# Kernel tuning notes

Hardware: AMD Instinct MI355X
Metric: run time of the kernel (lower is better)

The kernel has to match this reference:

```python
import jax, jax.numpy as jnp
import numpy as np

N = 4096        # batch size (rows)
K = 4           # instances per class -> num_instances in the torch code
D = 256         # embedding dim
MARGIN = 0.5
SAMPLE_KEY = jax.random.key(42)  # fixed key: deterministic stand-in for torch.multinomial


def setup_inputs() -> dict:
    key = jax.random.key(0)
    x = jax.random.normal(key, (N, D), dtype=jnp.float32)
    # L2-normalize like typical metric-learning embeddings so sims are in [-1, 1]
    inputs = x / jnp.linalg.norm(x, axis=1, keepdims=True)
    targets = (jnp.arange(N) // K).astype(jnp.int32)  # P*K batch: equal-size classes
    return {"inputs": inputs, "targets": targets}


def reference(inputs, targets):
    n = inputs.shape[0]
    km1 = K - 1                 # positives per row
    n_neg = n - K               # negatives per row

    sim = inputs @ inputs.T                                   # [n, n]
    same = targets[:, None] == targets[None, :]
    eye = jnp.eye(n, dtype=bool)
    pos_mask = same & ~eye
    neg_mask = ~same

    # masked_select + per-row sort: masked entries -> +inf, ascending sort,
    # keep first count entries (counts are uniform across rows)
    pos_sorted = jnp.sort(jnp.where(pos_mask, sim, jnp.inf), axis=1)[:, :km1]   # [n, K-1]
    neg_sorted = jnp.sort(jnp.where(neg_mask, sim, jnp.inf), axis=1)[:, :n_neg] # [n, n-K]

    pos_d = jnp.mean(pos_sorted)
    neg_d = jnp.mean(neg_sorted)

    # GaussDistribution per row over negatives
    neg_mean = jnp.mean(neg_sorted, axis=1, keepdims=True)
    neg_std = jnp.sqrt(jnp.mean((neg_sorted - neg_mean) ** 2, axis=1, keepdims=True))
    # NOTE: the original uses exp(+(x-mu)^2 / (2 sigma^2)) (no minus sign) -- faithful
    logprob = (neg_sorted - neg_mean) ** 2 / (2.0 * neg_std ** 2)               # [n, n-K]

    # multinomial without replacement ~ Gumbel top-k on log-weights
    gumbel = -jnp.log(-jnp.log(
        jax.random.uniform(SAMPLE_KEY, logprob.shape, minval=1e-20, maxval=1.0)))
    _, neg_idx = jax.lax.top_k(logprob + gumbel, km1)                            # [n, K-1]
    neg_pair = jnp.take_along_axis(neg_sorted, neg_idx, axis=1)                  # [n, K-1]

    pos_loss = jnp.mean(jnp.log1p(jnp.exp(-2.0 * (pos_sorted - MARGIN))), axis=1)
    neg_loss = 0.04 * jnp.mean(jnp.log1p(jnp.exp(50.0 * (neg_pair - MARGIN))), axis=1)
    loss = jnp.sum(pos_loss + neg_loss) / n

    # prec: fraction of rows where hardest positive > hardest sampled negative + 0.05
    c = jnp.sum(pos_sorted[:, -1] > jnp.max(neg_pair, axis=1) + 0.05)
    prec = c.astype(jnp.float32) / n

    return loss, prec, pos_d, neg_d
```

## Files before the change

kernel.cpp:

```cpp
#include <hip/hip_runtime.h>
#include <hip/hip_bf16.h>
#include <cstdint>
#include <cfloat>
#include <math.h>

#define NN 4096
#define DD 256
#define NNEG 4092
#define MARGIN 0.5f
#define NB 3584
#define NW (NB / 2)
#define GTOTAL ((uint32_t)NN * (uint32_t)NNEG)

__device__ __forceinline__ uint32_t rotl32(uint32_t x, int r) {
  return (x << r) | (x >> (32 - r));
}

__device__ __forceinline__ void threefry2x32_42(uint32_t x0, uint32_t x1,
                                                uint32_t& o0, uint32_t& o1) {
  const uint32_t k0 = 0u, k1 = 42u;
  const uint32_t k2 = k0 ^ k1 ^ 0x1BD11BDAu;
  x0 += k0; x1 += k1;
#define TF_R(r) { x0 += x1; x1 = rotl32(x1, r); x1 ^= x0; }
  TF_R(13) TF_R(15) TF_R(26) TF_R(6)
  x0 += k1; x1 += k2 + 1u;
  TF_R(17) TF_R(29) TF_R(16) TF_R(24)
  x0 += k2; x1 += k0 + 2u;
  TF_R(13) TF_R(15) TF_R(26) TF_R(6)
  x0 += k0; x1 += k1 + 3u;
  TF_R(17) TF_R(29) TF_R(16) TF_R(24)
  x0 += k1; x1 += k2 + 4u;
  TF_R(13) TF_R(15) TF_R(26) TF_R(6)
  x0 += k2; x1 += k0 + 5u;
#undef TF_R
  o0 = x0; o1 = x1;
}

__device__ __forceinline__ float gumbel_at(uint32_t f) {
  uint32_t o0, o1;
  threefry2x32_42(0u, f, o0, o1);
  uint32_t bits = o0 ^ o1;
  uint32_t fb = (bits >> 9) | 0x3F800000u;
  float fl = __uint_as_float(fb) - 1.0f;
  float u = fmaxf(1e-20f, fl + 1e-20f);
  return -logf(-logf(u));
}

__device__ __forceinline__ int bucket_of(float v) {
  return (int)fminf(fmaxf((v + 0.28f) * 6400.0f, 0.0f), (float)(NB - 1));
}

#define BT 64
#define NTT (NN / BT)
#define GEMM_BLOCKS (NTT * (NTT + 1) / 2)
#define BK 64
#define LDSS 68
#define GUMBEL_BLOCKS 384

template <int GOFF>
__global__ __launch_bounds__(256) void gemm_gumbel(const float* __restrict__ X,
                                                   float* __restrict__ S,
                                                   float* __restrict__ G) {
  __shared__ float As[BT * LDSS];
  __shared__ float Bs[BT * LDSS];
  const int tid = threadIdx.x;

  if (GOFF > 0 && (int)blockIdx.x < GOFF) {
    uint32_t i = (uint32_t)blockIdx.x * 256u + (uint32_t)tid;
    const uint32_t stride = (uint32_t)GOFF * 256u;
    for (; i < GTOTAL; i += stride) G[i] = gumbel_at(i);
    return;
  }

  const int tx = tid & 15, ty = tid >> 4;

  int b = (int)blockIdx.x - GOFF, bi = 0;
  while (b >= NTT - bi) { b -= NTT - bi; bi++; }
  const int bj = bi + b;
  const int rowBase = bi * BT, colBase = bj * BT;

  float acc[4][4] = {};
  for (int kb = 0; kb < DD; kb += BK) {
#pragma unroll
    for (int it = 0; it < 4; ++it) {
      int idx = tid + 256 * it;
      int r = idx >> 4, c4 = idx & 15;
      float4 av = *(const float4*)(X + (size_t)(rowBase + r) * DD + kb + c4 * 4);
      float4 bv = *(const float4*)(X + (size_t)(colBase + r) * DD + kb + c4 * 4);
      *(float4*)(As + r * LDSS + c4 * 4) = av;
      *(float4*)(Bs + r * LDSS + c4 * 4) = bv;
    }
    __syncthreads();
    for (int k = 0; k < BK; k += 4) {
      float4 a[4], bfr[4];
#pragma unroll
      for (int i = 0; i < 4; ++i) a[i] = *(const float4*)(As + (ty + 16 * i) * LDSS + k);
#pragma unroll
      for (int j = 0; j < 4; ++j) bfr[j] = *(const float4*)(Bs + (tx + 16 * j) * LDSS + k);
#pragma unroll
      for (int i = 0; i < 4; ++i)
#pragma unroll
        for (int j = 0; j < 4; ++j) {
          acc[i][j] += a[i].x * bfr[j].x;
          acc[i][j] += a[i].y * bfr[j].y;
          acc[i][j] += a[i].z * bfr[j].z;
          acc[i][j] += a[i].w * bfr[j].w;
        }
    }
    __syncthreads();
  }
#pragma unroll
  for (int i = 0; i < 4; ++i)
#pragma unroll
    for (int j = 0; j < 4; ++j)
      S[(size_t)(rowBase + ty + 16 * i) * NN + colBase + tx + 16 * j] = acc[i][j];
  if (bi != bj) {
#pragma unroll
    for (int i = 0; i < 4; ++i)
#pragma unroll
      for (int j = 0; j < 4; ++j)
        S[(size_t)(colBase + tx + 16 * j) * NN + rowBase + ty + 16 * i] = acc[i][j];
  }
}

#define INSERT3(sc, v)                                              \
  if ((sc) > s2) {                                                  \
    if ((sc) > s1) {                                                \
      s2 = s1; v2 = v1;                                             \
      if ((sc) > s0) { s1 = s0; v1 = v0; s0 = (sc); v0 = (v); }     \
      else           { s1 = (sc); v1 = (v); }                       \
    } else { s2 = (sc); v2 = (v); }                                 \
  }

template <int USE_G>
__global__ __launch_bounds__(256) void row_kernel(const float* __restrict__ S,
                                                  const float* __restrict__ G,
                                                  float* __restrict__ acc) {
  __shared__ uint32_t histw[NW];
  __shared__ uint32_t offsw[NW];
  __shared__ __align__(16) float sval[NN];
  __shared__ float sh[48];
  __shared__ uint32_t wtot[4];

  const int row = blockIdx.x;
  const int tid = threadIdx.x;
  const int lane = tid & 63, wid = tid >> 6;

#pragma unroll
  for (int i = 0; i < 7; ++i) histw[tid + 256 * i] = 0u;

  const float4* src = (const float4*)(S + (size_t)row * NN);
  const int pslot = row >> 2;
  float vv[16];
#pragma unroll
  for (int it = 0; it < 4; ++it) {
    int slot = tid + 256 * it;
    float4 t4 = src[slot];
    if (slot == pslot) {
      sh[16] = t4.x; sh[17] = t4.y; sh[18] = t4.z; sh[19] = t4.w;
      t4.x = INFINITY; t4.y = INFINITY; t4.z = INFINITY; t4.w = INFINITY;
    }
    vv[4 * it + 0] = t4.x; vv[4 * it + 1] = t4.y;
    vv[4 * it + 2] = t4.z; vv[4 * it + 3] = t4.w;
  }

  float s = 0.0f;
#pragma unroll
  for (int e = 0; e < 16; ++e) if (vv[e] < 1e30f) s += vv[e];
#pragma unroll
  for (int off = 32; off > 0; off >>= 1) s += __shfl_down(s, off, 64);
  if (lane == 0) sh[5 + wid] = s;
  __syncthreads();

#pragma unroll
  for (int e = 0; e < 16; ++e) {
    int b = bucket_of(vv[e]);
    atomicAdd(&histw[b >> 1], 1u << ((b & 1) << 4));
  }
  if (tid == 0) {
    int self = row & 3;
    float p[3]; int m = 0;
#pragma unroll
    for (int c = 0; c < 4; ++c)
      if (c != self) p[m++] = sh[16 + c];
    float t;
    if (p[0] > p[1]) { t = p[0]; p[0] = p[1]; p[1] = t; }
    if (p[1] > p[2]) { t = p[1]; p[1] = p[2]; p[2] = t; }
    if (p[0] > p[1]) { t = p[0]; p[0] = p[1]; p[1] = t; }
    sh[0] = p[0]; sh[1] = p[1]; sh[2] = p[2];
    float tot = sh[5] + sh[6] + sh[7] + sh[8];
    sh[9] = tot;
    sh[3] = tot / (float)NNEG;
  }
  __syncthreads();

  uint32_t hw[7];
  uint32_t s14 = 0;
#pragma unroll
  for (int j = 0; j < 7; ++j) {
    hw[j] = histw[7 * tid + j];
    s14 += (hw[j] & 0xFFFFu) + (hw[j] >> 16);
  }
  uint32_t inc = s14;
#pragma unroll
  for (int off = 1; off < 64; off <<= 1) {
    uint32_t n = __shfl_up(inc, (unsigned)off, 64);
    if (lane >= off) inc += n;
  }
  if (lane == 63) wtot[wid] = inc;

  const float mu = sh[3];
  float q = 0.0f;
#pragma unroll
  for (int e = 0; e < 16; ++e)
    if (vv[e] < 1e30f) { float d = vv[e] - mu; q += d * d; }
#pragma unroll
  for (int off = 32; off > 0; off >>= 1) q += __shfl_down(q, off, 64);
  if (lane == 0) sh[10 + wid] = q;
  __syncthreads();

  uint32_t wbase = 0;
  for (int w = 0; w < wid; ++w) wbase += wtot[w];
  uint32_t run = wbase + inc - s14;
#pragma unroll
  for (int j = 0; j < 7; ++j) {
    uint32_t lo = run; run += hw[j] & 0xFFFFu;
    uint32_t hi = run; run += hw[j] >> 16;
    offsw[7 * tid + j] = lo | (hi << 16);
  }
  if (tid == 0) {
    float var = (sh[10] + sh[11] + sh[12] + sh[13]) / (float)NNEG;
    float sd = sqrtf(var);
    sh[4] = 1.0f / (2.0f * sd * sd);
  }
  __syncthreads();

#pragma unroll
  for (int e = 0; e < 16; ++e) {
    int b = bucket_of(vv[e]);
    uint32_t old = atomicAdd(&offsw[b >> 1], 1u << ((b & 1) << 4));
    uint32_t sl = (old >> ((b & 1) << 4)) & 0xFFFFu;
    sval[sl] = vv[e];
  }
  __syncthreads();

  const float inv2s2 = sh[4];
  const uint32_t fbase = (uint32_t)row * (uint32_t)NNEG;
  const float* __restrict__ Grow = G + fbase;
  float s0 = -FLT_MAX, s1 = -FLT_MAX, s2 = -FLT_MAX;
  float v0 = 0.0f, v1 = 0.0f, v2 = 0.0f;

  float va[16]; uint32_t sten[16];
#pragma unroll
  for (int it = 0; it < 16; ++it) va[it] = sval[tid + 256 * it];
#pragma unroll
  for (int it = 0; it < 16; ++it) {
    float v = va[it];
    uint32_t pk = 0u;
    if (v < 1e30f) {
      int b = bucket_of(v);
      uint32_t sh16 = (uint32_t)((b & 1) << 4);
      uint32_t end = (offsw[b >> 1] >> sh16) & 0xFFFFu;
      uint32_t cb = (histw[b >> 1] >> sh16) & 0xFFFFu;
      pk = (end - cb) | (end << 16);
    }
    sten[it] = pk;
  }

#pragma unroll
  for (int half = 0; half < 2; ++half) {
    float4 w0[8];
#pragma unroll
    for (int j = 0; j < 8; ++j) {
      uint32_t st = sten[half * 8 + j] & 0xFFFFu;
      w0[j] = *(const float4*)(sval + (st & ~3u));
    }
#pragma unroll
    for (int j = 0; j < 8; ++j) {
      const int it = half * 8 + j;
      float v = va[it];
      if (v < 1e30f) {
        const int sl = tid + 256 * it;
        const uint32_t st = sten[it] & 0xFFFFu, en = sten[it] >> 16;
        const uint32_t nb = en - st;
        const uint32_t u0 = st & ~3u;
        int cnt = (int)st;
        {
          float4 w = w0[j];
          cnt += ((u0 + 0 - st) < nb && (w.x < v || (w.x == v && (int)(u0 + 0) < sl))) ? 1 : 0;
          cnt += ((u0 + 1 - st) < nb && (w.y < v || (w.y == v && (int)(u0 + 1) < sl))) ? 1 : 0;
          cnt += ((u0 + 2 - st) < nb && (w.z < v || (w.z == v && (int)(u0 + 2) < sl))) ? 1 : 0;
          cnt += ((u0 + 3 - st) < nb && (w.w < v || (w.w == v && (int)(u0 + 3) < sl))) ? 1 : 0;
        }
        for (uint32_t u = u0 + 4; u < en; u += 4) {
          float4 w = *(const float4*)(sval + u);
          cnt += ((u + 0 - st) < nb && (w.x < v || (w.x == v && (int)(u + 0) < sl))) ? 1 : 0;
          cnt += ((u + 1 - st) < nb && (w.y < v || (w.y == v && (int)(u + 1) < sl))) ? 1 : 0;
          cnt += ((u + 2 - st) < nb && (w.z < v || (w.z == v && (int)(u + 2) < sl))) ? 1 : 0;
          cnt += ((u + 3 - st) < nb && (w.w < v || (w.w == v && (int)(u + 3) < sl))) ? 1 : 0;
        }
        float g = USE_G ? Grow[cnt] : gumbel_at(fbase + (uint32_t)cnt);
        float d = v - mu;
        float sc = d * d * inv2s2 + g;
        INSERT3(sc, v)
      }
    }
  }

#pragma unroll
  for (int dlt = 1; dlt < 64; dlt <<= 1) {
    float t0 = __shfl_xor(s0, dlt, 64), u0 = __shfl_xor(v0, dlt, 64);
    float t1 = __shfl_xor(s1, dlt, 64), u1 = __shfl_xor(v1, dlt, 64);
    float t2 = __shfl_xor(s2, dlt, 64), u2 = __shfl_xor(v2, dlt, 64);
    INSERT3(t0, u0)
    INSERT3(t1, u1)
    INSERT3(t2, u2)
  }
  if (lane == 0) {
    int b0 = 24 + wid * 6;
    sh[b0 + 0] = s0; sh[b0 + 1] = v0;
    sh[b0 + 2] = s1; sh[b0 + 3] = v1;
    sh[b0 + 4] = s2; sh[b0 + 5] = v2;
  }
  __syncthreads();

  if (tid == 0) {
    float g0 = -FLT_MAX, g1 = -FLT_MAX, g2 = -FLT_MAX;
    float w0 = 0.0f, w1 = 0.0f, w2 = 0.0f;
    {
      float s0 = g0, s1 = g1, s2 = g2, v0 = w0, v1 = w1, v2 = w2;
#pragma unroll
      for (int i = 0; i < 12; ++i) {
        float sc = sh[24 + 2 * i], v = sh[24 + 2 * i + 1];
        INSERT3(sc, v)
      }
      g0 = s0; g1 = s1; g2 = s2; w0 = v0; w1 = v1; w2 = v2;
    }
    float negmax = fmaxf(w0, fmaxf(w1, w2));
    float neg_loss = 0.04f * (log1pf(expf(50.0f * (w0 - MARGIN))) +
                              log1pf(expf(50.0f * (w1 - MARGIN))) +
                              log1pf(expf(50.0f * (w2 - MARGIN)))) / 3.0f;
    float p0 = sh[0], p1 = sh[1], p2 = sh[2];
    float pos_loss = (log1pf(expf(-2.0f * (p0 - MARGIN))) +
                      log1pf(expf(-2.0f * (p1 - MARGIN))) +
                      log1pf(expf(-2.0f * (p2 - MARGIN)))) / 3.0f;
    atomicAdd(&acc[0], pos_loss + neg_loss);
    if (p2 > negmax + 0.05f) atomicAdd(&acc[1], 1.0f);
    atomicAdd(&acc[2], p0 + p1 + p2);
    atomicAdd(&acc[3], sh[9]);
  }
}

__global__ void finalize(const float* __restrict__ acc, float* out) {
  if (threadIdx.x == 0 && blockIdx.x == 0) {
    out[0] = acc[0] / 4096.0f;
    out[1] = acc[1] / 4096.0f;
    out[2] = acc[2] / (4096.0f * 3.0f);
    out[3] = acc[3] / (4096.0f * 4092.0f);
  }
}

extern "C" void kernel_launch(void* const* d_in, const int* in_sizes, int n_in,
                              void* d_out, int out_size, void* d_ws, size_t ws_size,
                              hipStream_t stream) {
  (void)in_sizes; (void)n_in; (void)out_size;
  const float* X = (const float*)d_in[0];
  float* S = (float*)d_ws;
  float* acc = (float*)((char*)d_ws + (size_t)NN * NN * 4);
  float* G = (float*)((char*)d_ws + (size_t)NN * NN * 4 + 256);
  const size_t need = (size_t)NN * NN * 4 + 256 + (size_t)GTOTAL * 4;
  const bool have_g = ws_size >= need;

  hipMemsetAsync(acc, 0, 4 * sizeof(float), stream);
  if (have_g) {
    gemm_gumbel<GUMBEL_BLOCKS><<<GUMBEL_BLOCKS + GEMM_BLOCKS, 256, 0, stream>>>(X, S, G);
    row_kernel<1><<<NN, 256, 0, stream>>>(S, G, acc);
  } else {
    gemm_gumbel<0><<<GEMM_BLOCKS, 256, 0, stream>>>(X, S, G);
    row_kernel<0><<<NN, 256, 0, stream>>>(S, G, acc);
  }
  finalize<<<1, 64, 0, stream>>>(acc, (float*)d_out);
}
```

Measured before the change: 375.0 us.

## Enlarge GEMM tiles to 128x128 and optionally move row sort buffer to global

Retiles the similarity GEMM to 128x128 blocks with a K-step of 32 and an 8x8 per-thread register tile. This cuts the number of blocks and the global reloads of X per output, and the Gumbel-generation blocks are moved after the GEMM blocks. The row kernel can now place its bucket-sorted value buffer in a per-row global workspace instead of LDS when the workspace is large enough. That frees about 16KB of LDS per block to allow higher occupancy, at the cost of scattered writes and repeated reads going through the cache hierarchy. The larger register tile raises register pressure in the GEMM.

```diff
diff --git a/kernel.cpp b/kernel.cpp
--- a/kernel.cpp
+++ b/kernel.cpp
@@ -50,12 +50,12 @@
   return (int)fminf(fmaxf((v + 0.28f) * 6400.0f, 0.0f), (float)(NB - 1));
 }
 
-#define BT 64
-#define NTT (NN / BT)
-#define GEMM_BLOCKS (NTT * (NTT + 1) / 2)
-#define BK 64
-#define LDSS 68
-#define GUMBEL_BLOCKS 384
+#define BT 128
+#define NT (NN / BT)
+#define BK 32
+#define LDSS 36
+#define GEMM_BLOCKS (NT * (NT + 1) / 2)
+#define GUMBEL_BLOCKS 240
 
 template <int GOFF>
 __global__ __launch_bounds__(256) void gemm_gumbel(const float* __restrict__ X,
@@ -65,8 +65,8 @@
   __shared__ float Bs[BT * LDSS];
   const int tid = threadIdx.x;
 
-  if (GOFF > 0 && (int)blockIdx.x < GOFF) {
-    uint32_t i = (uint32_t)blockIdx.x * 256u + (uint32_t)tid;
+  if (GOFF > 0 && (int)blockIdx.x >= GEMM_BLOCKS) {
+    uint32_t i = (uint32_t)(blockIdx.x - GEMM_BLOCKS) * 256u + (uint32_t)tid;
     const uint32_t stride = (uint32_t)GOFF * 256u;
     for (; i < GTOTAL; i += stride) G[i] = gumbel_at(i);
     return;
@@ -74,17 +74,17 @@
 
   const int tx = tid & 15, ty = tid >> 4;
 
-  int b = (int)blockIdx.x - GOFF, bi = 0;
-  while (b >= NTT - bi) { b -= NTT - bi; bi++; }
+  int b = blockIdx.x, bi = 0;
+  while (b >= NT - bi) { b -= NT - bi; bi++; }
   const int bj = bi + b;
   const int rowBase = bi * BT, colBase = bj * BT;
 
-  float acc[4][4] = {};
+  float acc[8][8] = {};
   for (int kb = 0; kb < DD; kb += BK) {
 #pragma unroll
     for (int it = 0; it < 4; ++it) {
       int idx = tid + 256 * it;
-      int r = idx >> 4, c4 = idx & 15;
+      int r = idx >> 3, c4 = idx & 7;
       float4 av = *(const float4*)(X + (size_t)(rowBase + r) * DD + kb + c4 * 4);
       float4 bv = *(const float4*)(X + (size_t)(colBase + r) * DD + kb + c4 * 4);
       *(float4*)(As + r * LDSS + c4 * 4) = av;
@@ -92,15 +92,15 @@
     }
     __syncthreads();
     for (int k = 0; k < BK; k += 4) {
-      float4 a[4], bfr[4];
-#pragma unroll
-      for (int i = 0; i < 4; ++i) a[i] = *(const float4*)(As + (ty + 16 * i) * LDSS + k);
-#pragma unroll
-      for (int j = 0; j < 4; ++j) bfr[j] = *(const float4*)(Bs + (tx + 16 * j) * LDSS + k);
-#pragma unroll
-      for (int i = 0; i < 4; ++i)
-#pragma unroll
-        for (int j = 0; j < 4; ++j) {
+      float4 a[8], bfr[8];
+#pragma unroll
+      for (int i = 0; i < 8; ++i) a[i] = *(const float4*)(As + (ty + 16 * i) * LDSS + k);
+#pragma unroll
+      for (int j = 0; j < 8; ++j) bfr[j] = *(const float4*)(Bs + (tx + 16 * j) * LDSS + k);
+#pragma unroll
+      for (int i = 0; i < 8; ++i)
+#pragma unroll
+        for (int j = 0; j < 8; ++j) {
           acc[i][j] += a[i].x * bfr[j].x;
           acc[i][j] += a[i].y * bfr[j].y;
           acc[i][j] += a[i].z * bfr[j].z;
@@ -110,15 +110,15 @@
     __syncthreads();
   }
 #pragma unroll
-  for (int i = 0; i < 4; ++i)
-#pragma unroll
-    for (int j = 0; j < 4; ++j)
+  for (int i = 0; i < 8; ++i)
+#pragma unroll
+    for (int j = 0; j < 8; ++j)
       S[(size_t)(rowBase + ty + 16 * i) * NN + colBase + tx + 16 * j] = acc[i][j];
   if (bi != bj) {
 #pragma unroll
-    for (int i = 0; i < 4; ++i)
-#pragma unroll
-      for (int j = 0; j < 4; ++j)
+    for (int i = 0; i < 8; ++i)
+#pragma unroll
+      for (int j = 0; j < 8; ++j)
         S[(size_t)(colBase + tx + 16 * j) * NN + rowBase + ty + 16 * i] = acc[i][j];
   }
 }
@@ -132,19 +132,22 @@
     } else { s2 = (sc); v2 = (v); }                                 \
   }
 
-template <int USE_G>
+template <int USE_G, int GSV>
 __global__ __launch_bounds__(256) void row_kernel(const float* __restrict__ S,
                                                   const float* __restrict__ G,
+                                                  float* __restrict__ svg,
                                                   float* __restrict__ acc) {
   __shared__ uint32_t histw[NW];
   __shared__ uint32_t offsw[NW];
-  __shared__ __align__(16) float sval[NN];
+  __shared__ __align__(16) float svs[GSV ? 4 : NN];
   __shared__ float sh[48];
   __shared__ uint32_t wtot[4];
 
   const int row = blockIdx.x;
   const int tid = threadIdx.x;
   const int lane = tid & 63, wid = tid >> 6;
+
+  float* __restrict__ sv = GSV ? (svg + ((size_t)row << 12)) : svs;
 
 #pragma unroll
   for (int i = 0; i < 7; ++i) histw[tid + 256 * i] = 0u;
@@ -240,7 +243,7 @@
     int b = bucket_of(vv[e]);
     uint32_t old = atomicAdd(&offsw[b >> 1], 1u << ((b & 1) << 4));
     uint32_t sl = (old >> ((b & 1) << 4)) & 0xFFFFu;
-    sval[sl] = vv[e];
+    sv[sl] = vv[e];
   }
   __syncthreads();
 
@@ -252,7 +255,7 @@
 
   float va[16]; uint32_t sten[16];
 #pragma unroll
-  for (int it = 0; it < 16; ++it) va[it] = sval[tid + 256 * it];
+  for (int it = 0; it < 16; ++it) va[it] = sv[tid + 256 * it];
 #pragma unroll
   for (int it = 0; it < 16; ++it) {
     float v = va[it];
@@ -273,7 +276,7 @@
 #pragma unroll
     for (int j = 0; j < 8; ++j) {
       uint32_t st = sten[half * 8 + j] & 0xFFFFu;
-      w0[j] = *(const float4*)(sval + (st & ~3u));
+      w0[j] = *(const float4*)(sv + (st & ~3u));
     }
 #pragma unroll
     for (int j = 0; j < 8; ++j) {
@@ -293,7 +296,7 @@
           cnt += ((u0 + 3 - st) < nb && (w.w < v || (w.w == v && (int)(u0 + 3) < sl))) ? 1 : 0;
         }
         for (uint32_t u = u0 + 4; u < en; u += 4) {
-          float4 w = *(const float4*)(sval + u);
+          float4 w = *(const float4*)(sv + u);
           cnt += ((u + 0 - st) < nb && (w.x < v || (w.x == v && (int)(u + 0) < sl))) ? 1 : 0;
           cnt += ((u + 1 - st) < nb && (w.y < v || (w.y == v && (int)(u + 1) < sl))) ? 1 : 0;
           cnt += ((u + 2 - st) < nb && (w.z < v || (w.z == v && (int)(u + 2) < sl))) ? 1 : 0;
@@ -368,16 +371,20 @@
   float* S = (float*)d_ws;
   float* acc = (float*)((char*)d_ws + (size_t)NN * NN * 4);
   float* G = (float*)((char*)d_ws + (size_t)NN * NN * 4 + 256);
-  const size_t need = (size_t)NN * NN * 4 + 256 + (size_t)GTOTAL * 4;
-  const bool have_g = ws_size >= need;
+  float* SV = (float*)((char*)d_ws + 2 * (size_t)NN * NN * 4 + 256);
+  const size_t need_g = (size_t)NN * NN * 4 + 256 + (size_t)GTOTAL * 4;
+  const size_t need_sv = 2 * (size_t)NN * NN * 4 + 256 + (size_t)NN * NN * 4;
+  const bool have_g = ws_size >= need_g;
+  const bool have_sv = ws_size >= need_sv;
 
   hipMemsetAsync(acc, 0, 4 * sizeof(float), stream);
   if (have_g) {
-    gemm_gumbel<GUMBEL_BLOCKS><<<GUMBEL_BLOCKS + GEMM_BLOCKS, 256, 0, stream>>>(X, S, G);
-    row_kernel<1><<<NN, 256, 0, stream>>>(S, G, acc);
+    gemm_gumbel<GUMBEL_BLOCKS><<<GEMM_BLOCKS + GUMBEL_BLOCKS, 256, 0, stream>>>(X, S, G);
+    if (have_sv) row_kernel<1, 1><<<NN, 256, 0, stream>>>(S, G, SV, acc);
+    else         row_kernel<1, 0><<<NN, 256, 0, stream>>>(S, G, SV, acc);
   } else {
     gemm_gumbel<0><<<GEMM_BLOCKS, 256, 0, stream>>>(X, S, G);
-    row_kernel<0><<<NN, 256, 0, stream>>>(S, G, acc);
+    row_kernel<0, 0><<<NN, 256, 0, stream>>>(S, G, SV, acc);
   }
   finalize<<<1, 64, 0, stream>>>(acc, (float*)d_out);
 }
```

Result: slower. 403.4 us (+7.6%).
